# Kernel optimization log

Hardware: AMD Instinct MI355X
Metric: run time of the kernel (lower is better)

The kernel has to match this reference:

```python
import jax, jax.numpy as jnp
import numpy as np

B, C = 512, 100000
MARGIN = 0.5
S = 64.0
ALPHA = 0.1  # weight on the noisy-margin branch


def setup_inputs() -> dict:
    key = jax.random.key(0)
    k1, k2, k3 = jax.random.split(key, 3)
    costh = jax.random.uniform(k1, (B, C), jnp.float32, minval=-0.99, maxval=0.99)
    eps = jax.random.normal(k2, (B, C), jnp.float32)  # standard normal, reparameterized noise
    label = jax.random.randint(k3, (B,), 0, C, jnp.int64)
    return {"costh": costh, "eps": eps, "label": label}


def reference(costh, eps, label):
    rows = jnp.arange(costh.shape[0])
    theta = jnp.arccos(costh)                       # [B, C]
    pos_theta = theta[rows, label]                  # [B]
    center_mean = jnp.mean(pos_theta)
    center_std = jnp.std(pos_theta, ddof=1)         # torch .std() is unbiased
    # torch.normal(mean, std, size) reparameterized; zero at the label column
    delt_mm = (center_mean + center_std * eps).at[rows, label].set(0.0)
    costh_mm = jnp.cos(theta - delt_mm)
    # additive margin only at the label column
    costh_pm = jnp.cos(theta.at[rows, label].add(MARGIN))
    costh_m = (ALPHA * costh_mm + costh_pm) / (1.0 + ALPHA)
    logits = S * costh_m
    logp = jax.nn.log_softmax(logits, axis=1)
    loss = -jnp.mean(logp[rows, label])
    return loss
```

## Files before the change

kernel.cpp:

```cpp
#include <hip/hip_runtime.h>
#include <math.h>

#define BB 512
#define CC 100000

#define K_MAIN 83.93862056f
#define K_MM   8.393862056f
#define K_BIAS -92.33248262f
#define COS05  0.8775825618903728f
#define SIN05  0.479425538604203f
#define SCALE  58.18181818f
#define INV_B  (1.0f / 512.0f)


__global__ __launch_bounds__(512) void stats_kernel(
    const float* __restrict__ costh, const float* __restrict__ eps,
    const int* __restrict__ label, float* __restrict__ ws,
    float* __restrict__ out) {
  const int b = threadIdx.x;
  if (b == 0) *out = 0.0f;
  const int lab = label[b];
  const float cth = costh[(size_t)b * CC + lab];
  const float ep  = eps[(size_t)b * CC + lab];
  const float th  = acosf(cth);

  __shared__ float red[8];
  __shared__ float s_mean, s_std;
  const int wave = b >> 6, lane = b & 63;

  float v = th;
  #pragma unroll
  for (int o = 32; o > 0; o >>= 1) v += __shfl_down(v, o, 64);
  if (lane == 0) red[wave] = v;
  __syncthreads();
  if (b == 0) {
    float s = 0.0f;
    #pragma unroll
    for (int i = 0; i < 8; i++) s += red[i];
    s_mean = s * INV_B;
  }
  __syncthreads();
  const float mean = s_mean;

  const float d = th - mean;
  v = d * d;
  #pragma unroll
  for (int o = 32; o > 0; o >>= 1) v += __shfl_down(v, o, 64);
  __syncthreads();
  if (lane == 0) red[wave] = v;
  __syncthreads();
  if (b == 0) {
    float s = 0.0f;
    #pragma unroll
    for (int i = 0; i < 8; i++) s += red[i];
    s_std = sqrtf(s / 511.0f);
    ws[0] = mean;
    ws[1] = s_std;
  }
  __syncthreads();
  const float stdv = s_std;

  const float sinth = sqrtf(fmaxf(fmaf(-cth, cth, 1.0f), 0.0f));
  const float cpm = fmaf(cth, COS05, -sinth * SIN05);
  const float logit_lab = SCALE * fmaf(0.1f, cth, cpm);
  const float arg_lab = fmaf(K_MM, cth, fmaf(K_MAIN, cpm, K_BIAS));

  const float delt = fmaf(stdv, ep, mean);
  float sd, cd;
  __sincosf(delt, &sd, &cd);
  const float cmm = fmaf(cth, cd, sinth * sd);
  const float arg_plain = fmaf(K_MM, cmm, fmaf(K_MAIN, cth, K_BIAS));

  ws[2 + b]   = __builtin_amdgcn_exp2f(arg_lab) - __builtin_amdgcn_exp2f(arg_plain);
  ws[514 + b] = logit_lab;
}

__device__ __forceinline__ float elem_exp(float cth, float ep, float mean, float stdv) {
  const float sinth = sqrtf(fmaxf(fmaf(-cth, cth, 1.0f), 0.0f));
  const float delt = fmaf(stdv, ep, mean);
  float sd, cd;
  __sincosf(delt, &sd, &cd);
  const float cmm = fmaf(cth, cd, sinth * sd);
  const float arg = fmaf(K_MM, cmm, fmaf(K_MAIN, cth, K_BIAS));
  return __builtin_amdgcn_exp2f(arg);
}

__device__ __forceinline__ float elem_exp4(float4 c, float4 e, float mean, float stdv) {
  return elem_exp(c.x, e.x, mean, stdv) + elem_exp(c.y, e.y, mean, stdv) +
         elem_exp(c.z, e.z, mean, stdv) + elem_exp(c.w, e.w, mean, stdv);
}

__global__ __launch_bounds__(1024) void main_kernel(
    const float* __restrict__ costh, const float* __restrict__ eps,
    const float* __restrict__ ws, float* __restrict__ out) {
  const int b = blockIdx.x;
  const float4* __restrict__ c4 = (const float4*)(costh + (size_t)b * CC);
  const float4* __restrict__ e4 = (const float4*)(eps + (size_t)b * CC);
  const float mean = ws[0];
  const float stdv = ws[1];

  float acc = 0.0f;
  int v = threadIdx.x;
  #pragma unroll 1
  for (int it = 0; it < 6; ++it, v += 4096) {
    const float4 c0 = c4[v];
    const float4 c1 = c4[v + 1024];
    const float4 c2 = c4[v + 2048];
    const float4 c3 = c4[v + 3072];
    const float4 e0 = e4[v];
    const float4 e1 = e4[v + 1024];
    const float4 e2 = e4[v + 2048];
    const float4 e3 = e4[v + 3072];
    acc += elem_exp4(c0, e0, mean, stdv);
    acc += elem_exp4(c1, e1, mean, stdv);
    acc += elem_exp4(c2, e2, mean, stdv);
    acc += elem_exp4(c3, e3, mean, stdv);
  }
  if (v < 25000) {
    const float4 c = c4[v];
    const float4 e = e4[v];
    acc += elem_exp4(c, e, mean, stdv);
  }

  #pragma unroll
  for (int o = 32; o > 0; o >>= 1) acc += __shfl_down(acc, o, 64);
  __shared__ float red[16];
  const int wave = threadIdx.x >> 6, lane = threadIdx.x & 63;
  if (lane == 0) red[wave] = acc;
  __syncthreads();
  if (threadIdx.x == 0) {
    float total = ws[2 + b];
    #pragma unroll
    for (int i = 0; i < 16; i++) total += red[i];
    const float loss_b = 64.0f + __logf(total) - ws[514 + b];
    atomicAdd(out, loss_b * INV_B);
  }
}

extern "C" void kernel_launch(void* const* d_in, const int* in_sizes, int n_in,
                              void* d_out, int out_size, void* d_ws, size_t ws_size,
                              hipStream_t stream) {
  const float* costh = (const float*)d_in[0];
  const float* eps   = (const float*)d_in[1];
  const int*   label = (const int*)d_in[2];
  float* out = (float*)d_out;
  float* ws  = (float*)d_ws;

  stats_kernel<<<1, 512, 0, stream>>>(costh, eps, label, ws, out);
  main_kernel<<<BB, 1024, 0, stream>>>(costh, eps, ws, out);
}
```

Before: 409.7 us.

## Software-pipeline row loads with register double buffering and occupancy hint

Restructures the main loop to prefetch the next pair of float4 chunks of costh and eps before computing on the current pair, with a scheduling barrier so the loads are issued early. It also adds a minimum-blocks occupancy hint to launch_bounds and drops the clamp before sqrt. The intent is better overlap of memory latency with the trig and exp math. The risk is register pressure or spills from the occupancy hint, and fewer loads in flight per iteration than the old four-way batch.

```diff
diff --git a/kernel.cpp b/kernel.cpp
--- a/kernel.cpp
+++ b/kernel.cpp
@@ -60,7 +60,7 @@
   __syncthreads();
   const float stdv = s_std;
 
-  const float sinth = sqrtf(fmaxf(fmaf(-cth, cth, 1.0f), 0.0f));
+  const float sinth = sqrtf(fmaf(-cth, cth, 1.0f));
   const float cpm = fmaf(cth, COS05, -sinth * SIN05);
   const float logit_lab = SCALE * fmaf(0.1f, cth, cpm);
   const float arg_lab = fmaf(K_MM, cth, fmaf(K_MAIN, cpm, K_BIAS));
@@ -76,7 +76,7 @@
 }
 
 __device__ __forceinline__ float elem_exp(float cth, float ep, float mean, float stdv) {
-  const float sinth = sqrtf(fmaxf(fmaf(-cth, cth, 1.0f), 0.0f));
+  const float sinth = sqrtf(fmaf(-cth, cth, 1.0f));
   const float delt = fmaf(stdv, ep, mean);
   float sd, cd;
   __sincosf(delt, &sd, &cd);
@@ -90,7 +90,7 @@
          elem_exp(c.z, e.z, mean, stdv) + elem_exp(c.w, e.w, mean, stdv);
 }
 
-__global__ __launch_bounds__(1024) void main_kernel(
+__global__ __launch_bounds__(1024, 4) void main_kernel(
     const float* __restrict__ costh, const float* __restrict__ eps,
     const float* __restrict__ ws, float* __restrict__ out) {
   const int b = blockIdx.x;
@@ -101,21 +101,29 @@
 
   float acc = 0.0f;
   int v = threadIdx.x;
+
+  float4 c0 = c4[v];
+  float4 c1 = c4[v + 1024];
+  float4 e0 = e4[v];
+  float4 e1 = e4[v + 1024];
+
   #pragma unroll 1
-  for (int it = 0; it < 6; ++it, v += 4096) {
-    const float4 c0 = c4[v];
-    const float4 c1 = c4[v + 1024];
-    const float4 c2 = c4[v + 2048];
-    const float4 c3 = c4[v + 3072];
-    const float4 e0 = e4[v];
-    const float4 e1 = e4[v + 1024];
-    const float4 e2 = e4[v + 2048];
-    const float4 e3 = e4[v + 3072];
+  for (int it = 0; it < 11; ++it) {
+    const int nv = v + 2048;
+    const float4 nc0 = c4[nv];
+    const float4 nc1 = c4[nv + 1024];
+    const float4 ne0 = e4[nv];
+    const float4 ne1 = e4[nv + 1024];
+    __builtin_amdgcn_sched_barrier(0);
     acc += elem_exp4(c0, e0, mean, stdv);
     acc += elem_exp4(c1, e1, mean, stdv);
-    acc += elem_exp4(c2, e2, mean, stdv);
-    acc += elem_exp4(c3, e3, mean, stdv);
+    c0 = nc0; c1 = nc1; e0 = ne0; e1 = ne1;
+    v = nv;
   }
+  acc += elem_exp4(c0, e0, mean, stdv);
+  acc += elem_exp4(c1, e1, mean, stdv);
+
+  v += 2048;
   if (v < 25000) {
     const float4 c = c4[v];
     const float4 e = e4[v];
```

Result: no change. 406.9 us (-0.7%).
